# Kernel optimization log

Hardware: AMD Instinct MI355X
Metric: run time of the kernel (lower is better)

The kernel has to match this reference:

```python
import jax, jax.numpy as jnp
import numpy as np

EMBED = 512
NH = 8
HD = EMBED // NH
NL = 12
FFN = 2048
TD = 16  # latent_channels * patch_size**2 = 4*4


def _ln(x, g, b):
    m = x.mean(-1, keepdims=True)
    v = ((x - m) ** 2).mean(-1, keepdims=True)
    return (x - m) * jax.lax.rsqrt(v + 1e-5) * g + b


def _pos_emb(H, W, d):
    # faithful to get_2d_rope_embedding: cosine 1D embeddings along h and w, concatenated
    dh = d // 2
    inv = 1.0 / (10000.0 ** (jnp.arange(dh, dtype=jnp.float32) / dh))
    peh = jnp.cos(jnp.arange(H, dtype=jnp.float32)[:, None] * inv[None, :])  # (H, dh)
    pew = jnp.cos(jnp.arange(W, dtype=jnp.float32)[:, None] * inv[None, :])  # (W, dh)
    pe = jnp.concatenate([
        jnp.broadcast_to(peh[:, None, :], (H, W, dh)),
        jnp.broadcast_to(pew[None, :, :], (H, W, dh)),
    ], axis=-1)
    return pe.reshape(H * W, d)


def setup_inputs() -> dict:
    key = jax.random.key(0)
    ks = jax.random.split(key, 20)
    B, L = 8, 1024
    s = 0.02
    inp = {
        'x': jax.random.normal(ks[0], (B, L, TD), jnp.float32),
        'token_mask': jnp.ones((B, L), jnp.int32),
        'W_in': s * jax.random.normal(ks[1], (TD, EMBED), jnp.float32),
        'b_in': jnp.zeros((EMBED,), jnp.float32),
        'ln1_g': jnp.ones((NL, EMBED), jnp.float32),
        'ln1_b': jnp.zeros((NL, EMBED), jnp.float32),
        'Wq': s * jax.random.normal(ks[2], (NL, EMBED, EMBED), jnp.float32),
        'Wk': s * jax.random.normal(ks[3], (NL, EMBED, EMBED), jnp.float32),
        'Wv': s * jax.random.normal(ks[4], (NL, EMBED, EMBED), jnp.float32),
        'Wo': s * jax.random.normal(ks[5], (NL, EMBED, EMBED), jnp.float32),
        'ln2_g': jnp.ones((NL, EMBED), jnp.float32),
        'ln2_b': jnp.zeros((NL, EMBED), jnp.float32),
        'W1': s * jax.random.normal(ks[6], (NL, EMBED, FFN), jnp.float32),
        'W2': s * jax.random.normal(ks[7], (NL, EMBED, FFN), jnp.float32),
        'W3': s * jax.random.normal(ks[8], (NL, FFN, EMBED), jnp.float32),
        'W_out': s * jax.random.normal(ks[9], (EMBED, TD), jnp.float32),
        'b_out': jnp.zeros((TD,), jnp.float32),
        'H': 32,
        'W': 32,
    }
    return inp


def reference(x, token_mask, W_in, b_in, ln1_g, ln1_b, Wq, Wk, Wv, Wo,
              ln2_g, ln2_b, W1, W2, W3, W_out, b_out, H, W):
    B, L, _ = x.shape
    scale = 1.0 / np.sqrt(HD).astype(np.float32)
    h = x @ W_in + b_in + _pos_emb(H, W, EMBED)[None]  # (B, L, E)
    # (B,1,1,L) additive mask, -1e9 at padded positions
    mask = (token_mask == 0)[:, None, None, :].astype(h.dtype) * (-1e9)

    def block(h, p):
        g1, b1, wq, wk, wv, wo, g2, b2, w1, w2, w3 = p
        xn = _ln(h, g1, b1)
        q = (xn @ wq).reshape(B, L, NH, HD)
        k = (xn @ wk).reshape(B, L, NH, HD)
        v = (xn @ wv).reshape(B, L, NH, HD)
        s = jnp.einsum('blhd,bmhd->bhlm', q, k) * scale + mask
        a = jax.nn.softmax(s, axis=-1)
        o = jnp.einsum('bhlm,bmhd->blhd', a, v).reshape(B, L, EMBED) @ wo
        h = h + o
        xn = _ln(h, g2, b2)
        h = h + (jax.nn.silu(xn @ w1) * (xn @ w2)) @ w3
        return h, None

    h, _ = jax.lax.scan(block, h, (ln1_g, ln1_b, Wq, Wk, Wv, Wo, ln2_g, ln2_b, W1, W2, W3))
    return h @ W_out + b_out  # (B, L, TD)
```

## Files before the change

kernel.cpp:

```cpp
#include <hip/hip_runtime.h>

typedef __attribute__((ext_vector_type(8))) short short8;
typedef __attribute__((ext_vector_type(4))) float f32x4;
typedef __attribute__((ext_vector_type(4))) unsigned short us4;

#define MFMA_BF16(a,b,c) __builtin_amdgcn_mfma_f32_16x16x32_bf16((a),(b),(c),0,0,0)

__device__ __forceinline__ unsigned short f2bf(float f) {
  unsigned int u = __float_as_uint(f);
  u += 0x7fffu + ((u >> 16) & 1u);
  return (unsigned short)(u >> 16);
}

__global__ __launch_bounds__(256) void wtrans_kernel(const float* __restrict__ src,
                                                     unsigned short* __restrict__ dst,
                                                     int R, int C) {
  __shared__ float tile[32][33];
  int c0 = blockIdx.x * 32, r0 = blockIdx.y * 32;
  const float* s = src + (size_t)blockIdx.z * R * C;
  unsigned short* d = dst + (size_t)blockIdx.z * R * C;
  int tx = threadIdx.x, ty = threadIdx.y;
#pragma unroll
  for (int i = 0; i < 32; i += 8)
    tile[ty + i][tx] = s[(size_t)(r0 + ty + i) * C + c0 + tx];
  __syncthreads();
#pragma unroll
  for (int i = 0; i < 32; i += 8)
    d[(size_t)(c0 + ty + i) * R + r0 + tx] = f2bf(tile[tx][ty + i]);
}

__global__ __launch_bounds__(128) void embed_kernel(const float* __restrict__ x,
                                                    const float* __restrict__ Win,
                                                    const float* __restrict__ bin,
                                                    float* __restrict__ h) {
  __shared__ float xs[16];
  int m = blockIdx.x, t = threadIdx.x;
  if (t < 16) xs[t] = x[m * 16 + t];
  __syncthreads();
  int l = m & 1023, hi = l >> 5, wi = l & 31;
#pragma unroll
  for (int e0 = 0; e0 < 512; e0 += 128) {
    int e = e0 + t;
    float a = bin[e];
#pragma unroll
    for (int kk = 0; kk < 16; kk++) a += xs[kk] * Win[kk * 512 + e];
    int j = e & 255;
    float p = (e < 256) ? (float)hi : (float)wi;
    float inv = expf((float)j * (-9.210340371976184f / 256.0f));
    a += cosf(p * inv);
    h[(size_t)m * 512 + e] = a;
  }
}

__global__ __launch_bounds__(128) void ln_kernel(const float* __restrict__ h,
                                                 const float* __restrict__ gw,
                                                 const float* __restrict__ bw,
                                                 unsigned short* __restrict__ xn) {
  int m = blockIdx.x, t = threadIdx.x;
  f32x4 v = *(const f32x4*)&h[(size_t)m * 512 + t * 4];
  float s = v[0] + v[1] + v[2] + v[3];
  float q = v[0]*v[0] + v[1]*v[1] + v[2]*v[2] + v[3]*v[3];
#pragma unroll
  for (int o = 1; o < 64; o <<= 1) { s += __shfl_xor(s, o); q += __shfl_xor(q, o); }
  __shared__ float red[4];
  if ((t & 63) == 0) { red[(t >> 6) * 2] = s; red[(t >> 6) * 2 + 1] = q; }
  __syncthreads();
  s = red[0] + red[2]; q = red[1] + red[3];
  float mean = s * (1.0f / 512.0f);
  float var = q * (1.0f / 512.0f) - mean * mean;
  float rstd = rsqrtf(var + 1e-5f);
  f32x4 gg = *(const f32x4*)&gw[t * 4];
  f32x4 bb = *(const f32x4*)&bw[t * 4];
  us4 w;
#pragma unroll
  for (int r = 0; r < 4; r++) w[r] = f2bf((v[r] - mean) * rstd * gg[r] + bb[r]);
  *(us4*)&xn[(size_t)m * 512 + t * 4] = w;
}

__global__ __launch_bounds__(256) void qkv_gemm(const unsigned short* __restrict__ xn,
                                                const unsigned short* __restrict__ wtq,
                                                const unsigned short* __restrict__ wtk,
                                                const unsigned short* __restrict__ wtv,
                                                unsigned short* __restrict__ qo,
                                                unsigned short* __restrict__ ko,
                                                unsigned short* __restrict__ vo) {
  __shared__ short8 As[512];
  __shared__ short8 Bs[512];
  int n0 = blockIdx.x * 128, m0 = blockIdx.y * 128;
  int sel = n0 >> 9;
  const short8* wt = (const short8*)(sel == 0 ? wtq : sel == 1 ? wtk : wtv);
  unsigned short* out = sel == 0 ? qo : sel == 1 ? ko : vo;
  int nw = n0 & 511;
  const short8* A8 = (const short8*)xn;
  int tid = threadIdx.x, wid = tid >> 6, lane = tid & 63;
  int wr = wid >> 1, wc = wid & 1, c16 = lane & 15, g = lane >> 4;
  int subA = wid * 2;
  f32x4 acc[4][4] = {};
  short8 ra[2], rb[2];
#pragma unroll
  for (int s = 0; s < 2; s++) {
    ra[s] = A8[(size_t)(m0 + (subA + s) * 16 + c16) * 64 + g];
    rb[s] = wt[(size_t)(nw + (subA + s) * 16 + c16) * 64 + g];
  }
  for (int kt = 0; kt < 16; kt++) {
    __syncthreads();
#pragma unroll
    for (int s = 0; s < 2; s++) {
      As[(subA + s) * 64 + lane] = ra[s];
      Bs[(subA + s) * 64 + lane] = rb[s];
    }
    if (kt < 15) {
#pragma unroll
      for (int s = 0; s < 2; s++) {
        ra[s] = A8[(size_t)(m0 + (subA + s) * 16 + c16) * 64 + (kt + 1) * 4 + g];
        rb[s] = wt[(size_t)(nw + (subA + s) * 16 + c16) * 64 + (kt + 1) * 4 + g];
      }
    }
    __syncthreads();
    short8 af[4], bf[4];
#pragma unroll
    for (int mf = 0; mf < 4; mf++) af[mf] = As[(wr * 4 + mf) * 64 + lane];
#pragma unroll
    for (int nf = 0; nf < 4; nf++) bf[nf] = Bs[(wc * 4 + nf) * 64 + lane];
#pragma unroll
    for (int mf = 0; mf < 4; mf++)
#pragma unroll
      for (int nf = 0; nf < 4; nf++)
        acc[mf][nf] = MFMA_BF16(af[mf], bf[nf], acc[mf][nf]);
  }
#pragma unroll
  for (int mf = 0; mf < 4; mf++)
#pragma unroll
    for (int nf = 0; nf < 4; nf++) {
      int col = nw + wc * 64 + nf * 16 + c16;
#pragma unroll
      for (int r = 0; r < 4; r++) {
        int row = m0 + wr * 64 + mf * 16 + g * 4 + r;
        out[(size_t)row * 512 + col] = f2bf(acc[mf][nf][r]);
      }
    }
}

__global__ __launch_bounds__(256) void gemm_res(const unsigned short* __restrict__ A,
                                                const unsigned short* __restrict__ Wt,
                                                float* __restrict__ h, int Kd8, int nkt) {
  __shared__ short8 As[512];
  __shared__ short8 Bs[512];
  int n0 = blockIdx.x * 128, m0 = blockIdx.y * 128;
  const short8* A8 = (const short8*)A;
  const short8* W8 = (const short8*)Wt;
  int tid = threadIdx.x, wid = tid >> 6, lane = tid & 63;
  int wr = wid >> 1, wc = wid & 1, c16 = lane & 15, g = lane >> 4;
  int subA = wid * 2;
  f32x4 acc[4][4] = {};
  short8 ra[2], rb[2];
#pragma unroll
  for (int s = 0; s < 2; s++) {
    ra[s] = A8[(size_t)(m0 + (subA + s) * 16 + c16) * Kd8 + g];
    rb[s] = W8[(size_t)(n0 + (subA + s) * 16 + c16) * Kd8 + g];
  }
  for (int kt = 0; kt < nkt; kt++) {
    __syncthreads();
#pragma unroll
    for (int s = 0; s < 2; s++) {
      As[(subA + s) * 64 + lane] = ra[s];
      Bs[(subA + s) * 64 + lane] = rb[s];
    }
    if (kt + 1 < nkt) {
#pragma unroll
      for (int s = 0; s < 2; s++) {
        ra[s] = A8[(size_t)(m0 + (subA + s) * 16 + c16) * Kd8 + (kt + 1) * 4 + g];
        rb[s] = W8[(size_t)(n0 + (subA + s) * 16 + c16) * Kd8 + (kt + 1) * 4 + g];
      }
    }
    __syncthreads();
    short8 af[4], bf[4];
#pragma unroll
    for (int mf = 0; mf < 4; mf++) af[mf] = As[(wr * 4 + mf) * 64 + lane];
#pragma unroll
    for (int nf = 0; nf < 4; nf++) bf[nf] = Bs[(wc * 4 + nf) * 64 + lane];
#pragma unroll
    for (int mf = 0; mf < 4; mf++)
#pragma unroll
      for (int nf = 0; nf < 4; nf++)
        acc[mf][nf] = MFMA_BF16(af[mf], bf[nf], acc[mf][nf]);
  }
#pragma unroll
  for (int mf = 0; mf < 4; mf++)
#pragma unroll
    for (int nf = 0; nf < 4; nf++) {
      int col = n0 + wc * 64 + nf * 16 + c16;
#pragma unroll
      for (int r = 0; r < 4; r++) {
        int row = m0 + wr * 64 + mf * 16 + g * 4 + r;
        h[(size_t)row * 512 + col] += acc[mf][nf][r];
      }
    }
}

__global__ __launch_bounds__(256) void ffn_gemm(const unsigned short* __restrict__ xn,
                                                const unsigned short* __restrict__ w1t,
                                                const unsigned short* __restrict__ w2t,
                                                unsigned short* __restrict__ gout) {
  __shared__ short8 As[512];
  __shared__ short8 B1s[512];
  __shared__ short8 B2s[512];
  int n0 = blockIdx.x * 128, m0 = blockIdx.y * 128;
  const short8* A8 = (const short8*)xn;
  const short8* W18 = (const short8*)w1t;
  const short8* W28 = (const short8*)w2t;
  int tid = threadIdx.x, wid = tid >> 6, lane = tid & 63;
  int wr = wid >> 1, wc = wid & 1, c16 = lane & 15, g = lane >> 4;
  int subA = wid * 2;
  f32x4 acc1[4][4] = {};
  f32x4 acc2[4][4] = {};
  short8 ra[2], rb1[2], rb2[2];
#pragma unroll
  for (int s = 0; s < 2; s++) {
    ra[s]  = A8 [(size_t)(m0 + (subA + s) * 16 + c16) * 64 + g];
    rb1[s] = W18[(size_t)(n0 + (subA + s) * 16 + c16) * 64 + g];
    rb2[s] = W28[(size_t)(n0 + (subA + s) * 16 + c16) * 64 + g];
  }
  for (int kt = 0; kt < 16; kt++) {
    __syncthreads();
#pragma unroll
    for (int s = 0; s < 2; s++) {
      As [(subA + s) * 64 + lane] = ra[s];
      B1s[(subA + s) * 64 + lane] = rb1[s];
      B2s[(subA + s) * 64 + lane] = rb2[s];
    }
    if (kt < 15) {
#pragma unroll
      for (int s = 0; s < 2; s++) {
        ra[s]  = A8 [(size_t)(m0 + (subA + s) * 16 + c16) * 64 + (kt + 1) * 4 + g];
        rb1[s] = W18[(size_t)(n0 + (subA + s) * 16 + c16) * 64 + (kt + 1) * 4 + g];
        rb2[s] = W28[(size_t)(n0 + (subA + s) * 16 + c16) * 64 + (kt + 1) * 4 + g];
      }
    }
    __syncthreads();
    short8 af[4], b1f[4], b2f[4];
#pragma unroll
    for (int mf = 0; mf < 4; mf++) af[mf] = As[(wr * 4 + mf) * 64 + lane];
#pragma unroll
    for (int nf = 0; nf < 4; nf++) {
      b1f[nf] = B1s[(wc * 4 + nf) * 64 + lane];
      b2f[nf] = B2s[(wc * 4 + nf) * 64 + lane];
    }
#pragma unroll
    for (int mf = 0; mf < 4; mf++)
#pragma unroll
      for (int nf = 0; nf < 4; nf++) {
        acc1[mf][nf] = MFMA_BF16(af[mf], b1f[nf], acc1[mf][nf]);
        acc2[mf][nf] = MFMA_BF16(af[mf], b2f[nf], acc2[mf][nf]);
      }
  }
#pragma unroll
  for (int mf = 0; mf < 4; mf++)
#pragma unroll
    for (int nf = 0; nf < 4; nf++) {
      int col = n0 + wc * 64 + nf * 16 + c16;
#pragma unroll
      for (int r = 0; r < 4; r++) {
        int row = m0 + wr * 64 + mf * 16 + g * 4 + r;
        float xx = acc1[mf][nf][r];
        float yy = acc2[mf][nf][r];
        float sg = xx / (1.0f + __expf(-xx));
        gout[(size_t)row * 2048 + col] = f2bf(sg * yy);
      }
    }
}

__global__ __launch_bounds__(256) void vtrans_kernel(const unsigned short* __restrict__ v,
                                                     unsigned short* __restrict__ vt) {
  __shared__ __align__(16) unsigned short tile[64][72];
  int bid = blockIdx.x;
  int bh = bid >> 4, lt = bid & 15;
  int b = bh >> 3, hh = bh & 7;
  int t = threadIdx.x;
  int lr = t >> 2, d0 = (t & 3) * 16;
  const unsigned short* src = v + (size_t)(b * 1024 + lt * 64 + lr) * 512 + hh * 64 + d0;
  *(short8*)&tile[lr][d0] = *(const short8*)src;
  *(short8*)&tile[lr][d0 + 8] = *(const short8*)(src + 8);
  __syncthreads();
  int d = t & 63, l0 = (t >> 6) * 16;
  unsigned short* dst = vt + (size_t)(bh * 64 + d) * 1024 + lt * 64 + l0;
  short8 w0, w1;
#pragma unroll
  for (int i = 0; i < 8; i++) w0[i] = (short)tile[l0 + i][d];
#pragma unroll
  for (int i = 0; i < 8; i++) w1[i] = (short)tile[l0 + 8 + i][d];
  *(short8*)dst = w0;
  *(short8*)(dst + 8) = w1;
}

__global__ __launch_bounds__(256) void attn_kernel(const unsigned short* __restrict__ q,
                                                   const unsigned short* __restrict__ k,
                                                   const unsigned short* __restrict__ vt,
                                                   const int* __restrict__ tmsk,
                                                   unsigned short* __restrict__ o) {
  __shared__ short8 Ks[512];
  __shared__ short8 Vs[512];
  __shared__ uint2  Pb[2048];
  __shared__ f32x4  maskv[256];

  int bid = blockIdx.x;
  int qb = bid & 7;
  int bh = bid >> 3;
  int b = bh >> 3, hh = bh & 7;
  int tid = threadIdx.x, wid = tid >> 6, lane = tid & 63;
  int c16 = lane & 15, gq = lane >> 4;
  int qrow0 = qb * 128 + wid * 32;

  const short8* q8 = (const short8*)q;
  const short8* k8 = (const short8*)k;
  const short8* v8 = (const short8*)vt;

  short8 qf[2][2];
#pragma unroll
  for (int nf = 0; nf < 2; nf++)
#pragma unroll
    for (int dc = 0; dc < 2; dc++)
      qf[nf][dc] = q8[(size_t)(b * 1024 + qrow0 + nf * 16 + c16) * 64 + hh * 8 + dc * 4 + gq];

  {
    int4 mm = ((const int4*)(tmsk + b * 1024))[tid];
    f32x4 ma;
    ma[0] = (mm.x == 0) ? -1e9f : 0.0f;
    ma[1] = (mm.y == 0) ? -1e9f : 0.0f;
    ma[2] = (mm.z == 0) ? -1e9f : 0.0f;
    ma[3] = (mm.w == 0) ? -1e9f : 0.0f;
    maskv[tid] = ma;
  }

  short8 rk[2], rv[2];
#pragma unroll
  for (int s = 0; s < 2; s++) {
    int sub = wid * 2 + s;
    rk[s] = k8[(size_t)(b * 1024 + (sub >> 1) * 16 + c16) * 64 + hh * 8 + (sub & 1) * 4 + gq];
    rv[s] = v8[(size_t)(bh * 64 + (sub >> 1) * 16 + c16) * 128 + (sub & 1) * 4 + gq];
  }

  float mrun[2] = {-1e30f, -1e30f};
  float lrun[2] = {0.0f, 0.0f};
  f32x4 accO[4][2] = {};

  for (int kt = 0; kt < 16; kt++) {
    __syncthreads();
#pragma unroll
    for (int s = 0; s < 2; s++) {
      int sub = wid * 2 + s;
      Ks[sub * 64 + lane] = rk[s];
      Vs[sub * 64 + lane] = rv[s];
    }
    if (kt < 15) {
      int kt2 = kt + 1;
#pragma unroll
      for (int s = 0; s < 2; s++) {
        int sub = wid * 2 + s;
        rk[s] = k8[(size_t)(b * 1024 + kt2 * 64 + (sub >> 1) * 16 + c16) * 64 + hh * 8 + (sub & 1) * 4 + gq];
        rv[s] = v8[(size_t)(bh * 64 + (sub >> 1) * 16 + c16) * 128 + kt2 * 8 + (sub & 1) * 4 + gq];
      }
    }
    __syncthreads();

    f32x4 sT[4][2] = {};
#pragma unroll
    for (int mf = 0; mf < 4; mf++) {
      short8 ka0 = Ks[(mf * 2 + 0) * 64 + lane];
      short8 ka1 = Ks[(mf * 2 + 1) * 64 + lane];
#pragma unroll
      for (int nf = 0; nf < 2; nf++) {
        sT[mf][nf] = MFMA_BF16(ka0, qf[nf][0], sT[mf][nf]);
        sT[mf][nf] = MFMA_BF16(ka1, qf[nf][1], sT[mf][nf]);
      }
    }

#pragma unroll
    for (int nf = 0; nf < 2; nf++) {
      float pv[4][4];
      float tm = -1e30f;
#pragma unroll
      for (int mf = 0; mf < 4; mf++) {
        f32x4 mk = maskv[kt * 16 + mf * 4 + gq];
#pragma unroll
        for (int r = 0; r < 4; r++) {
          float sv = sT[mf][nf][r] * 0.125f + mk[r];
          pv[mf][r] = sv;
          tm = fmaxf(tm, sv);
        }
      }
      tm = fmaxf(tm, __shfl_xor(tm, 16));
      tm = fmaxf(tm, __shfl_xor(tm, 32));
      float mn = fmaxf(mrun[nf], tm);
      float fac = __expf(mrun[nf] - mn);
      mrun[nf] = mn;
      float ts = 0.0f;
#pragma unroll
      for (int mf = 0; mf < 4; mf++)
#pragma unroll
        for (int r = 0; r < 4; r++) {
          float p = __expf(pv[mf][r] - mn);
          pv[mf][r] = p;
          ts += p;
        }
      ts += __shfl_xor(ts, 16);
      ts += __shfl_xor(ts, 32);
      lrun[nf] = lrun[nf] * fac + ts;
#pragma unroll
      for (int dmf = 0; dmf < 4; dmf++) accO[dmf][nf] *= fac;
#pragma unroll
      for (int mf = 0; mf < 4; mf++) {
        unsigned lo = (unsigned)f2bf(pv[mf][0]) | ((unsigned)f2bf(pv[mf][1]) << 16);
        unsigned hi = (unsigned)f2bf(pv[mf][2]) | ((unsigned)f2bf(pv[mf][3]) << 16);
        int kk = mf >> 1;
        int gr = (mf & 1) * 2 + (gq >> 1);
        uint2 t2; t2.x = lo; t2.y = hi;
        Pb[wid * 512 + ((nf * 2 + kk) * 64 + gr * 16 + c16) * 2 + (gq & 1)] = t2;
      }
    }
    __syncthreads();

    const short8* Pb8 = (const short8*)Pb;
#pragma unroll
    for (int nf = 0; nf < 2; nf++) {
      short8 pb0 = Pb8[wid * 256 + (nf * 2 + 0) * 64 + lane];
      short8 pb1 = Pb8[wid * 256 + (nf * 2 + 1) * 64 + lane];
#pragma unroll
      for (int dmf = 0; dmf < 4; dmf++) {
        short8 va0 = Vs[(dmf * 2 + 0) * 64 + lane];
        short8 va1 = Vs[(dmf * 2 + 1) * 64 + lane];
        accO[dmf][nf] = MFMA_BF16(va0, pb0, accO[dmf][nf]);
        accO[dmf][nf] = MFMA_BF16(va1, pb1, accO[dmf][nf]);
      }
    }
  }

#pragma unroll
  for (int nf = 0; nf < 2; nf++) {
    float inv = 1.0f / lrun[nf];
    int row = b * 1024 + qrow0 + nf * 16 + c16;
#pragma unroll
    for (int dmf = 0; dmf < 4; dmf++) {
      us4 w;
#pragma unroll
      for (int r = 0; r < 4; r++) w[r] = f2bf(accO[dmf][nf][r] * inv);
      *(us4*)&o[(size_t)row * 512 + hh * 64 + dmf * 16 + gq * 4] = w;
    }
  }
}

__global__ __launch_bounds__(128) void out_kernel(const float* __restrict__ h,
                                                  const float* __restrict__ Wout,
                                                  const float* __restrict__ bout,
                                                  float* __restrict__ out) {
  __shared__ f32x4 hs4[8][128];
  __shared__ f32x4 Ws4[16][129];
  int t = threadIdx.x;
  int rb = blockIdx.x * 8;
  float* hsf = (float*)hs4;
  float* wsf = (float*)Ws4;
  for (int i = t; i < 4096; i += 128) hsf[i] = h[(size_t)rb * 512 + i];
  for (int i = t; i < 8192; i += 128) wsf[(i & 15) * 516 + (i >> 4)] = Wout[i];
  __syncthreads();
  int r = t >> 4, c = t & 15;
  float acc = bout[c];
  for (int k4 = 0; k4 < 128; k4++) {
    f32x4 a = hs4[r][k4];
    f32x4 w = Ws4[c][k4];
    acc += a[0]*w[0] + a[1]*w[1] + a[2]*w[2] + a[3]*w[3];
  }
  out[(rb + r) * 16 + c] = acc;
}

extern "C" void kernel_launch(void* const* d_in, const int* in_sizes, int n_in,
                              void* d_out, int out_size, void* d_ws, size_t ws_size,
                              hipStream_t stream) {
  const float* x    = (const float*)d_in[0];
  const int*   tmsk = (const int*)d_in[1];
  const float* Win  = (const float*)d_in[2];
  const float* bin  = (const float*)d_in[3];
  const float* ln1g = (const float*)d_in[4];
  const float* ln1b = (const float*)d_in[5];
  const float* Wq   = (const float*)d_in[6];
  const float* Wk   = (const float*)d_in[7];
  const float* Wv   = (const float*)d_in[8];
  const float* Wo   = (const float*)d_in[9];
  const float* ln2g = (const float*)d_in[10];
  const float* ln2b = (const float*)d_in[11];
  const float* W1   = (const float*)d_in[12];
  const float* W2   = (const float*)d_in[13];
  const float* W3   = (const float*)d_in[14];
  const float* Wout = (const float*)d_in[15];
  const float* bout = (const float*)d_in[16];
  float* outp = (float*)d_out;

  char* ws = (char*)d_ws;
  unsigned short* wtq = (unsigned short*)(ws + 0);
  unsigned short* wtk = (unsigned short*)(ws + 6291456);
  unsigned short* wtv = (unsigned short*)(ws + 12582912);
  unsigned short* wto = (unsigned short*)(ws + 18874368);
  unsigned short* wt1 = (unsigned short*)(ws + 25165824);
  unsigned short* wt2 = (unsigned short*)(ws + 50331648);
  unsigned short* wt3 = (unsigned short*)(ws + 75497472);
  float*          h   = (float*)(ws + 100663296);
  unsigned short* xn  = (unsigned short*)(ws + 117440512);
  unsigned short* qb  = (unsigned short*)(ws + 125829120);
  unsigned short* kb  = (unsigned short*)(ws + 134217728);
  unsigned short* vb  = (unsigned short*)(ws + 142606336);
  unsigned short* vtb = (unsigned short*)(ws + 150994944);
  unsigned short* ob  = (unsigned short*)(ws + 159383552);
  unsigned short* gb  = (unsigned short*)(ws + 167772160);

  dim3 tb(32, 8);
  wtrans_kernel<<<dim3(16, 16, 12), tb, 0, stream>>>(Wq, wtq, 512, 512);
  wtrans_kernel<<<dim3(16, 16, 12), tb, 0, stream>>>(Wk, wtk, 512, 512);
  wtrans_kernel<<<dim3(16, 16, 12), tb, 0, stream>>>(Wv, wtv, 512, 512);
  wtrans_kernel<<<dim3(16, 16, 12), tb, 0, stream>>>(Wo, wto, 512, 512);
  wtrans_kernel<<<dim3(64, 16, 12), tb, 0, stream>>>(W1, wt1, 512, 2048);
  wtrans_kernel<<<dim3(64, 16, 12), tb, 0, stream>>>(W2, wt2, 512, 2048);
  wtrans_kernel<<<dim3(16, 64, 12), tb, 0, stream>>>(W3, wt3, 2048, 512);

  embed_kernel<<<8192, 128, 0, stream>>>(x, Win, bin, h);

  for (int l = 0; l < 12; l++) {
    ln_kernel<<<8192, 128, 0, stream>>>(h, ln1g + l * 512, ln1b + l * 512, xn);
    qkv_gemm<<<dim3(12, 64), 256, 0, stream>>>(xn,
        wtq + (size_t)l * 262144, wtk + (size_t)l * 262144, wtv + (size_t)l * 262144,
        qb, kb, vb);
    vtrans_kernel<<<1024, 256, 0, stream>>>(vb, vtb);
    attn_kernel<<<512, 256, 0, stream>>>(qb, kb, vtb, tmsk, ob);
    gemm_res<<<dim3(4, 64), 256, 0, stream>>>(ob, wto + (size_t)l * 262144, h, 64, 16);
    ln_kernel<<<8192, 128, 0, stream>>>(h, ln2g + l * 512, ln2b + l * 512, xn);
    ffn_gemm<<<dim3(16, 64), 256, 0, stream>>>(xn,
        wt1 + (size_t)l * 1048576, wt2 + (size_t)l * 1048576, gb);
    gemm_res<<<dim3(4, 64), 256, 0, stream>>>(gb, wt3 + (size_t)l * 1048576, h, 256, 64);
  }
  out_kernel<<<1024, 128, 0, stream>>>(h, Wout, bout, outp);

  (void)in_sizes; (void)n_in; (void)out_size; (void)ws_size;
}
```

Baseline: 2.720 ms.

## Double-buffer GEMM tiles via direct global-to-LDS async loads

The three MFMA GEMM kernels (QKV, residual, FFN) now load tiles straight from global memory into LDS with global_load_lds, instead of staging them through registers. LDS is double-buffered so the next k-tile is fetched while the current one feeds the MFMAs. This cuts register staging and one barrier per iteration. In exchange it doubles LDS use, which may lower occupancy. It also relies on the compiler's waitcnt handling before each barrier to make the async LDS writes visible.

```diff
diff --git a/kernel.cpp b/kernel.cpp
--- a/kernel.cpp
+++ b/kernel.cpp
@@ -5,6 +5,13 @@
 typedef __attribute__((ext_vector_type(4))) unsigned short us4;
 
 #define MFMA_BF16(a,b,c) __builtin_amdgcn_mfma_f32_16x16x32_bf16((a),(b),(c),0,0,0)
+
+typedef __attribute__((address_space(3))) void* lds_vp;
+typedef const __attribute__((address_space(1))) void* gbl_vp;
+
+__device__ __forceinline__ void gl16(const void* g, void* l) {
+  __builtin_amdgcn_global_load_lds((gbl_vp)g, (lds_vp)l, 16, 0, 0);
+}
 
 __device__ __forceinline__ unsigned short f2bf(float f) {
   unsigned int u = __float_as_uint(f);
@@ -84,8 +91,8 @@
                                                 unsigned short* __restrict__ qo,
                                                 unsigned short* __restrict__ ko,
                                                 unsigned short* __restrict__ vo) {
-  __shared__ short8 As[512];
-  __shared__ short8 Bs[512];
+  __shared__ short8 As[2][512];
+  __shared__ short8 Bs[2][512];
   int n0 = blockIdx.x * 128, m0 = blockIdx.y * 128;
   int sel = n0 >> 9;
   const short8* wt = (const short8*)(sel == 0 ? wtq : sel == 1 ? wtk : wtv);
@@ -94,39 +101,39 @@
   const short8* A8 = (const short8*)xn;
   int tid = threadIdx.x, wid = tid >> 6, lane = tid & 63;
   int wr = wid >> 1, wc = wid & 1, c16 = lane & 15, g = lane >> 4;
-  int subA = wid * 2;
+  int sub0 = wid * 2, sub1 = wid * 2 + 1;
+  const short8* aS0 = A8 + (size_t)(m0 + sub0 * 16 + c16) * 64 + g;
+  const short8* aS1 = A8 + (size_t)(m0 + sub1 * 16 + c16) * 64 + g;
+  const short8* bS0 = wt + (size_t)(nw + sub0 * 16 + c16) * 64 + g;
+  const short8* bS1 = wt + (size_t)(nw + sub1 * 16 + c16) * 64 + g;
   f32x4 acc[4][4] = {};
-  short8 ra[2], rb[2];
-#pragma unroll
-  for (int s = 0; s < 2; s++) {
-    ra[s] = A8[(size_t)(m0 + (subA + s) * 16 + c16) * 64 + g];
-    rb[s] = wt[(size_t)(nw + (subA + s) * 16 + c16) * 64 + g];
-  }
+
+  gl16(aS0, &As[0][sub0 * 64]);
+  gl16(aS1, &As[0][sub1 * 64]);
+  gl16(bS0, &Bs[0][sub0 * 64]);
+  gl16(bS1, &Bs[0][sub1 * 64]);
+  __syncthreads();
+  int cur = 0;
   for (int kt = 0; kt < 16; kt++) {
-    __syncthreads();
-#pragma unroll
-    for (int s = 0; s < 2; s++) {
-      As[(subA + s) * 64 + lane] = ra[s];
-      Bs[(subA + s) * 64 + lane] = rb[s];
-    }
     if (kt < 15) {
-#pragma unroll
-      for (int s = 0; s < 2; s++) {
-        ra[s] = A8[(size_t)(m0 + (subA + s) * 16 + c16) * 64 + (kt + 1) * 4 + g];
-        rb[s] = wt[(size_t)(nw + (subA + s) * 16 + c16) * 64 + (kt + 1) * 4 + g];
-      }
-    }
-    __syncthreads();
+      int ko_ = (kt + 1) * 4;
+      gl16(aS0 + ko_, &As[cur ^ 1][sub0 * 64]);
+      gl16(aS1 + ko_, &As[cur ^ 1][sub1 * 64]);
+      gl16(bS0 + ko_, &Bs[cur ^ 1][sub0 * 64]);
+      gl16(bS1 + ko_, &Bs[cur ^ 1][sub1 * 64]);
+    }
     short8 af[4], bf[4];
 #pragma unroll
-    for (int mf = 0; mf < 4; mf++) af[mf] = As[(wr * 4 + mf) * 64 + lane];
-#pragma unroll
-    for (int nf = 0; nf < 4; nf++) bf[nf] = Bs[(wc * 4 + nf) * 64 + lane];
+    for (int mf = 0; mf < 4; mf++) af[mf] = As[cur][(wr * 4 + mf) * 64 + lane];
+#pragma unroll
+    for (int nf = 0; nf < 4; nf++) bf[nf] = Bs[cur][(wc * 4 + nf) * 64 + lane];
 #pragma unroll
     for (int mf = 0; mf < 4; mf++)
 #pragma unroll
       for (int nf = 0; nf < 4; nf++)
         acc[mf][nf] = MFMA_BF16(af[mf], bf[nf], acc[mf][nf]);
+    __syncthreads();
+    cur ^= 1;
   }
 #pragma unroll
   for (int mf = 0; mf < 4; mf++)
@@ -144,46 +151,46 @@
 __global__ __launch_bounds__(256) void gemm_res(const unsigned short* __restrict__ A,
                                                 const unsigned short* __restrict__ Wt,
                                                 float* __restrict__ h, int Kd8, int nkt) {
-  __shared__ short8 As[512];
-  __shared__ short8 Bs[512];
+  __shared__ short8 As[2][512];
+  __shared__ short8 Bs[2][512];
   int n0 = blockIdx.x * 128, m0 = blockIdx.y * 128;
   const short8* A8 = (const short8*)A;
   const short8* W8 = (const short8*)Wt;
   int tid = threadIdx.x, wid = tid >> 6, lane = tid & 63;
   int wr = wid >> 1, wc = wid & 1, c16 = lane & 15, g = lane >> 4;
-  int subA = wid * 2;
+  int sub0 = wid * 2, sub1 = wid * 2 + 1;
+  const short8* aS0 = A8 + (size_t)(m0 + sub0 * 16 + c16) * Kd8 + g;
+  const short8* aS1 = A8 + (size_t)(m0 + sub1 * 16 + c16) * Kd8 + g;
+  const short8* bS0 = W8 + (size_t)(n0 + sub0 * 16 + c16) * Kd8 + g;
+  const short8* bS1 = W8 + (size_t)(n0 + sub1 * 16 + c16) * Kd8 + g;
   f32x4 acc[4][4] = {};
-  short8 ra[2], rb[2];
-#pragma unroll
-  for (int s = 0; s < 2; s++) {
-    ra[s] = A8[(size_t)(m0 + (subA + s) * 16 + c16) * Kd8 + g];
-    rb[s] = W8[(size_t)(n0 + (subA + s) * 16 + c16) * Kd8 + g];
-  }
+
+  gl16(aS0, &As[0][sub0 * 64]);
+  gl16(aS1, &As[0][sub1 * 64]);
+  gl16(bS0, &Bs[0][sub0 * 64]);
+  gl16(bS1, &Bs[0][sub1 * 64]);
+  __syncthreads();
+  int cur = 0;
   for (int kt = 0; kt < nkt; kt++) {
-    __syncthreads();
-#pragma unroll
-    for (int s = 0; s < 2; s++) {
-      As[(subA + s) * 64 + lane] = ra[s];
-      Bs[(subA + s) * 64 + lane] = rb[s];
-    }
     if (kt + 1 < nkt) {
-#pragma unroll
-      for (int s = 0; s < 2; s++) {
-        ra[s] = A8[(size_t)(m0 + (subA + s) * 16 + c16) * Kd8 + (kt + 1) * 4 + g];
-        rb[s] = W8[(size_t)(n0 + (subA + s) * 16 + c16) * Kd8 + (kt + 1) * 4 + g];
-      }
-    }
-    __syncthreads();
+      int ko_ = (kt + 1) * 4;
+      gl16(aS0 + ko_, &As[cur ^ 1][sub0 * 64]);
+      gl16(aS1 + ko_, &As[cur ^ 1][sub1 * 64]);
+      gl16(bS0 + ko_, &Bs[cur ^ 1][sub0 * 64]);
+      gl16(bS1 + ko_, &Bs[cur ^ 1][sub1 * 64]);
+    }
     short8 af[4], bf[4];
 #pragma unroll
-    for (int mf = 0; mf < 4; mf++) af[mf] = As[(wr * 4 + mf) * 64 + lane];
-#pragma unroll
-    for (int nf = 0; nf < 4; nf++) bf[nf] = Bs[(wc * 4 + nf) * 64 + lane];
+    for (int mf = 0; mf < 4; mf++) af[mf] = As[cur][(wr * 4 + mf) * 64 + lane];
+#pragma unroll
+    for (int nf = 0; nf < 4; nf++) bf[nf] = Bs[cur][(wc * 4 + nf) * 64 + lane];
 #pragma unroll
     for (int mf = 0; mf < 4; mf++)
 #pragma unroll
       for (int nf = 0; nf < 4; nf++)
         acc[mf][nf] = MFMA_BF16(af[mf], bf[nf], acc[mf][nf]);
+    __syncthreads();
+    cur ^= 1;
   }
 #pragma unroll
   for (int mf = 0; mf < 4; mf++)
@@ -202,49 +209,50 @@
                                                 const unsigned short* __restrict__ w1t,
                                                 const unsigned short* __restrict__ w2t,
                                                 unsigned short* __restrict__ gout) {
-  __shared__ short8 As[512];
-  __shared__ short8 B1s[512];
-  __shared__ short8 B2s[512];
+  __shared__ short8 As[2][512];
+  __shared__ short8 B1s[2][512];
+  __shared__ short8 B2s[2][512];
   int n0 = blockIdx.x * 128, m0 = blockIdx.y * 128;
   const short8* A8 = (const short8*)xn;
   const short8* W18 = (const short8*)w1t;
   const short8* W28 = (const short8*)w2t;
   int tid = threadIdx.x, wid = tid >> 6, lane = tid & 63;
   int wr = wid >> 1, wc = wid & 1, c16 = lane & 15, g = lane >> 4;
-  int subA = wid * 2;
+  int sub0 = wid * 2, sub1 = wid * 2 + 1;
+  const short8* aS0 = A8 + (size_t)(m0 + sub0 * 16 + c16) * 64 + g;
+  const short8* aS1 = A8 + (size_t)(m0 + sub1 * 16 + c16) * 64 + g;
+  const short8* b1S0 = W18 + (size_t)(n0 + sub0 * 16 + c16) * 64 + g;
+  const short8* b1S1 = W18 + (size_t)(n0 + sub1 * 16 + c16) * 64 + g;
+  const short8* b2S0 = W28 + (size_t)(n0 + sub0 * 16 + c16) * 64 + g;
+  const short8* b2S1 = W28 + (size_t)(n0 + sub1 * 16 + c16) * 64 + g;
   f32x4 acc1[4][4] = {};
   f32x4 acc2[4][4] = {};
-  short8 ra[2], rb1[2], rb2[2];
-#pragma unroll
-  for (int s = 0; s < 2; s++) {
-    ra[s]  = A8 [(size_t)(m0 + (subA + s) * 16 + c16) * 64 + g];
-    rb1[s] = W18[(size_t)(n0 + (subA + s) * 16 + c16) * 64 + g];
-    rb2[s] = W28[(size_t)(n0 + (subA + s) * 16 + c16) * 64 + g];
-  }
+
+  gl16(aS0, &As[0][sub0 * 64]);
+  gl16(aS1, &As[0][sub1 * 64]);
+  gl16(b1S0, &B1s[0][sub0 * 64]);
+  gl16(b1S1, &B1s[0][sub1 * 64]);
+  gl16(b2S0, &B2s[0][sub0 * 64]);
+  gl16(b2S1, &B2s[0][sub1 * 64]);
+  __syncthreads();
+  int cur = 0;
   for (int kt = 0; kt < 16; kt++) {
-    __syncthreads();
-#pragma unroll
-    for (int s = 0; s < 2; s++) {
-      As [(subA + s) * 64 + lane] = ra[s];
-      B1s[(subA + s) * 64 + lane] = rb1[s];
-      B2s[(subA + s) * 64 + lane] = rb2[s];
-    }
     if (kt < 15) {
-#pragma unroll
-      for (int s = 0; s < 2; s++) {
-        ra[s]  = A8 [(size_t)(m0 + (subA + s) * 16 + c16) * 64 + (kt + 1) * 4 + g];
-        rb1[s] = W18[(size_t)(n0 + (subA + s) * 16 + c16) * 64 + (kt + 1) * 4 + g];
-        rb2[s] = W28[(size_t)(n0 + (subA + s) * 16 + c16) * 64 + (kt + 1) * 4 + g];
-      }
-    }
-    __syncthreads();
+      int ko_ = (kt + 1) * 4;
+      gl16(aS0 + ko_, &As[cur ^ 1][sub0 * 64]);
+      gl16(aS1 + ko_, &As[cur ^ 1][sub1 * 64]);
+      gl16(b1S0 + ko_, &B1s[cur ^ 1][sub0 * 64]);
+      gl16(b1S1 + ko_, &B1s[cur ^ 1][sub1 * 64]);
+      gl16(b2S0 + ko_, &B2s[cur ^ 1][sub0 * 64]);
+      gl16(b2S1 + ko_, &B2s[cur ^ 1][sub1 * 64]);
+    }
     short8 af[4], b1f[4], b2f[4];
 #pragma unroll
-    for (int mf = 0; mf < 4; mf++) af[mf] = As[(wr * 4 + mf) * 64 + lane];
+    for (int mf = 0; mf < 4; mf++) af[mf] = As[cur][(wr * 4 + mf) * 64 + lane];
 #pragma unroll
     for (int nf = 0; nf < 4; nf++) {
-      b1f[nf] = B1s[(wc * 4 + nf) * 64 + lane];
-      b2f[nf] = B2s[(wc * 4 + nf) * 64 + lane];
+      b1f[nf] = B1s[cur][(wc * 4 + nf) * 64 + lane];
+      b2f[nf] = B2s[cur][(wc * 4 + nf) * 64 + lane];
     }
 #pragma unroll
     for (int mf = 0; mf < 4; mf++)
@@ -253,6 +261,8 @@
         acc1[mf][nf] = MFMA_BF16(af[mf], b1f[nf], acc1[mf][nf]);
         acc2[mf][nf] = MFMA_BF16(af[mf], b2f[nf], acc2[mf][nf]);
       }
+    __syncthreads();
+    cur ^= 1;
   }
 #pragma unroll
   for (int mf = 0; mf < 4; mf++)
```

Result: slower. 3.053 ms (+12.2%).

## Use direct global-to-LDS loads with K=64 tiles and narrower residual GEMM tiles

Applied to the files above, without the earlier changes.

The three GEMM kernels now load tiles with global_load_lds straight into shared memory, skipping the register staging. The K tile doubles to 64, which halves the number of barrier pairs per K step. The residual GEMMs use 128x64 output tiles, doubling their grid to 512 blocks for better CU occupancy. The register prefetch overlap is dropped, so load latency is now exposed between barriers, and LDS use per block grows.

```diff
diff --git a/kernel.cpp b/kernel.cpp
--- a/kernel.cpp
+++ b/kernel.cpp
@@ -5,6 +5,13 @@
 typedef __attribute__((ext_vector_type(4))) unsigned short us4;
 
 #define MFMA_BF16(a,b,c) __builtin_amdgcn_mfma_f32_16x16x32_bf16((a),(b),(c),0,0,0)
+
+typedef __attribute__((address_space(3))) void* lds_vp;
+typedef const __attribute__((address_space(1))) void* gbl_vp;
+
+__device__ __forceinline__ void gl16(const void* g, void* l) {
+  __builtin_amdgcn_global_load_lds((gbl_vp)g, (lds_vp)l, 16, 0, 0);
+}
 
 __device__ __forceinline__ unsigned short f2bf(float f) {
   unsigned int u = __float_as_uint(f);
@@ -84,8 +91,8 @@
                                                 unsigned short* __restrict__ qo,
                                                 unsigned short* __restrict__ ko,
                                                 unsigned short* __restrict__ vo) {
-  __shared__ short8 As[512];
-  __shared__ short8 Bs[512];
+  __shared__ short8 As[1024];
+  __shared__ short8 Bs[1024];
   int n0 = blockIdx.x * 128, m0 = blockIdx.y * 128;
   int sel = n0 >> 9;
   const short8* wt = (const short8*)(sel == 0 ? wtq : sel == 1 ? wtk : wtv);
@@ -94,39 +101,36 @@
   const short8* A8 = (const short8*)xn;
   int tid = threadIdx.x, wid = tid >> 6, lane = tid & 63;
   int wr = wid >> 1, wc = wid & 1, c16 = lane & 15, g = lane >> 4;
-  int subA = wid * 2;
+  const short8* aSrc[4];
+  const short8* bSrc[4];
+#pragma unroll
+  for (int s = 0; s < 4; s++) {
+    int sub = wid * 4 + s, rg = sub >> 1, kc = sub & 1;
+    aSrc[s] = A8 + (size_t)(m0 + rg * 16 + c16) * 64 + kc * 4 + g;
+    bSrc[s] = wt + (size_t)(nw + rg * 16 + c16) * 64 + kc * 4 + g;
+  }
   f32x4 acc[4][4] = {};
-  short8 ra[2], rb[2];
-#pragma unroll
-  for (int s = 0; s < 2; s++) {
-    ra[s] = A8[(size_t)(m0 + (subA + s) * 16 + c16) * 64 + g];
-    rb[s] = wt[(size_t)(nw + (subA + s) * 16 + c16) * 64 + g];
-  }
-  for (int kt = 0; kt < 16; kt++) {
+  for (int kt = 0; kt < 8; kt++) {
+    if (kt) __syncthreads();
+#pragma unroll
+    for (int s = 0; s < 4; s++) {
+      gl16(aSrc[s] + kt * 8, &As[(wid * 4 + s) * 64]);
+      gl16(bSrc[s] + kt * 8, &Bs[(wid * 4 + s) * 64]);
+    }
     __syncthreads();
 #pragma unroll
-    for (int s = 0; s < 2; s++) {
-      As[(subA + s) * 64 + lane] = ra[s];
-      Bs[(subA + s) * 64 + lane] = rb[s];
-    }
-    if (kt < 15) {
-#pragma unroll
-      for (int s = 0; s < 2; s++) {
-        ra[s] = A8[(size_t)(m0 + (subA + s) * 16 + c16) * 64 + (kt + 1) * 4 + g];
-        rb[s] = wt[(size_t)(nw + (subA + s) * 16 + c16) * 64 + (kt + 1) * 4 + g];
-      }
-    }
-    __syncthreads();
-    short8 af[4], bf[4];
-#pragma unroll
-    for (int mf = 0; mf < 4; mf++) af[mf] = As[(wr * 4 + mf) * 64 + lane];
-#pragma unroll
-    for (int nf = 0; nf < 4; nf++) bf[nf] = Bs[(wc * 4 + nf) * 64 + lane];
-#pragma unroll
-    for (int mf = 0; mf < 4; mf++)
-#pragma unroll
-      for (int nf = 0; nf < 4; nf++)
-        acc[mf][nf] = MFMA_BF16(af[mf], bf[nf], acc[mf][nf]);
+    for (int kc = 0; kc < 2; kc++) {
+      short8 af[4], bf[4];
+#pragma unroll
+      for (int mf = 0; mf < 4; mf++) af[mf] = As[((wr * 4 + mf) * 2 + kc) * 64 + lane];
+#pragma unroll
+      for (int nf = 0; nf < 4; nf++) bf[nf] = Bs[((wc * 4 + nf) * 2 + kc) * 64 + lane];
+#pragma unroll
+      for (int mf = 0; mf < 4; mf++)
+#pragma unroll
+        for (int nf = 0; nf < 4; nf++)
+          acc[mf][nf] = MFMA_BF16(af[mf], bf[nf], acc[mf][nf]);
+    }
   }
 #pragma unroll
   for (int mf = 0; mf < 4; mf++)
@@ -144,52 +148,52 @@
 __global__ __launch_bounds__(256) void gemm_res(const unsigned short* __restrict__ A,
                                                 const unsigned short* __restrict__ Wt,
                                                 float* __restrict__ h, int Kd8, int nkt) {
-  __shared__ short8 As[512];
+  __shared__ short8 As[1024];
   __shared__ short8 Bs[512];
-  int n0 = blockIdx.x * 128, m0 = blockIdx.y * 128;
+  int n0 = blockIdx.x * 64, m0 = blockIdx.y * 128;
   const short8* A8 = (const short8*)A;
   const short8* W8 = (const short8*)Wt;
   int tid = threadIdx.x, wid = tid >> 6, lane = tid & 63;
   int wr = wid >> 1, wc = wid & 1, c16 = lane & 15, g = lane >> 4;
-  int subA = wid * 2;
-  f32x4 acc[4][4] = {};
-  short8 ra[2], rb[2];
+  const short8* aSrc[4];
+  const short8* bSrc[2];
+#pragma unroll
+  for (int s = 0; s < 4; s++) {
+    int sub = wid * 4 + s, rg = sub >> 1, kc = sub & 1;
+    aSrc[s] = A8 + (size_t)(m0 + rg * 16 + c16) * Kd8 + kc * 4 + g;
+  }
 #pragma unroll
   for (int s = 0; s < 2; s++) {
-    ra[s] = A8[(size_t)(m0 + (subA + s) * 16 + c16) * Kd8 + g];
-    rb[s] = W8[(size_t)(n0 + (subA + s) * 16 + c16) * Kd8 + g];
-  }
+    int sub = wid * 2 + s, rg = sub >> 1, kc = sub & 1;
+    bSrc[s] = W8 + (size_t)(n0 + rg * 16 + c16) * Kd8 + kc * 4 + g;
+  }
+  f32x4 acc[4][2] = {};
   for (int kt = 0; kt < nkt; kt++) {
+    if (kt) __syncthreads();
+#pragma unroll
+    for (int s = 0; s < 4; s++) gl16(aSrc[s] + kt * 8, &As[(wid * 4 + s) * 64]);
+#pragma unroll
+    for (int s = 0; s < 2; s++) gl16(bSrc[s] + kt * 8, &Bs[(wid * 2 + s) * 64]);
     __syncthreads();
 #pragma unroll
-    for (int s = 0; s < 2; s++) {
-      As[(subA + s) * 64 + lane] = ra[s];
-      Bs[(subA + s) * 64 + lane] = rb[s];
-    }
-    if (kt + 1 < nkt) {
-#pragma unroll
-      for (int s = 0; s < 2; s++) {
-        ra[s] = A8[(size_t)(m0 + (subA + s) * 16 + c16) * Kd8 + (kt + 1) * 4 + g];
-        rb[s] = W8[(size_t)(n0 + (subA + s) * 16 + c16) * Kd8 + (kt + 1) * 4 + g];
-      }
-    }
-    __syncthreads();
-    short8 af[4], bf[4];
-#pragma unroll
-    for (int mf = 0; mf < 4; mf++) af[mf] = As[(wr * 4 + mf) * 64 + lane];
-#pragma unroll
-    for (int nf = 0; nf < 4; nf++) bf[nf] = Bs[(wc * 4 + nf) * 64 + lane];
-#pragma unroll
-    for (int mf = 0; mf < 4; mf++)
-#pragma unroll
-      for (int nf = 0; nf < 4; nf++)
-        acc[mf][nf] = MFMA_BF16(af[mf], bf[nf], acc[mf][nf]);
+    for (int kc = 0; kc < 2; kc++) {
+      short8 af[4], bf[2];
+#pragma unroll
+      for (int mf = 0; mf < 4; mf++) af[mf] = As[((wr * 4 + mf) * 2 + kc) * 64 + lane];
+#pragma unroll
+      for (int nf = 0; nf < 2; nf++) bf[nf] = Bs[((wc * 2 + nf) * 2 + kc) * 64 + lane];
+#pragma unroll
+      for (int mf = 0; mf < 4; mf++)
+#pragma unroll
+        for (int nf = 0; nf < 2; nf++)
+          acc[mf][nf] = MFMA_BF16(af[mf], bf[nf], acc[mf][nf]);
+    }
   }
 #pragma unroll
   for (int mf = 0; mf < 4; mf++)
 #pragma unroll
-    for (int nf = 0; nf < 4; nf++) {
-      int col = n0 + wc * 64 + nf * 16 + c16;
+    for (int nf = 0; nf < 2; nf++) {
+      int col = n0 + wc * 32 + nf * 16 + c16;
 #pragma unroll
       for (int r = 0; r < 4; r++) {
         int row = m0 + wr * 64 + mf * 16 + g * 4 + r;
@@ -202,57 +206,54 @@
                                                 const unsigned short* __restrict__ w1t,
                                                 const unsigned short* __restrict__ w2t,
                                                 unsigned short* __restrict__ gout) {
-  __shared__ short8 As[512];
-  __shared__ short8 B1s[512];
-  __shared__ short8 B2s[512];
+  __shared__ short8 As[1024];
+  __shared__ short8 B1s[1024];
+  __shared__ short8 B2s[1024];
   int n0 = blockIdx.x * 128, m0 = blockIdx.y * 128;
   const short8* A8 = (const short8*)xn;
   const short8* W18 = (const short8*)w1t;
   const short8* W28 = (const short8*)w2t;
   int tid = threadIdx.x, wid = tid >> 6, lane = tid & 63;
   int wr = wid >> 1, wc = wid & 1, c16 = lane & 15, g = lane >> 4;
-  int subA = wid * 2;
+  const short8* aSrc[4];
+  const short8* b1Src[4];
+  const short8* b2Src[4];
+#pragma unroll
+  for (int s = 0; s < 4; s++) {
+    int sub = wid * 4 + s, rg = sub >> 1, kc = sub & 1;
+    aSrc[s]  = A8  + (size_t)(m0 + rg * 16 + c16) * 64 + kc * 4 + g;
+    b1Src[s] = W18 + (size_t)(n0 + rg * 16 + c16) * 64 + kc * 4 + g;
+    b2Src[s] = W28 + (size_t)(n0 + rg * 16 + c16) * 64 + kc * 4 + g;
+  }
   f32x4 acc1[4][4] = {};
   f32x4 acc2[4][4] = {};
-  short8 ra[2], rb1[2], rb2[2];
-#pragma unroll
-  for (int s = 0; s < 2; s++) {
-    ra[s]  = A8 [(size_t)(m0 + (subA + s) * 16 + c16) * 64 + g];
-    rb1[s] = W18[(size_t)(n0 + (subA + s) * 16 + c16) * 64 + g];
-    rb2[s] = W28[(size_t)(n0 + (subA + s) * 16 + c16) * 64 + g];
-  }
-  for (int kt = 0; kt < 16; kt++) {
+  for (int kt = 0; kt < 8; kt++) {
+    if (kt) __syncthreads();
+#pragma unroll
+    for (int s = 0; s < 4; s++) {
+      gl16(aSrc[s]  + kt * 8, &As [(wid * 4 + s) * 64]);
+      gl16(b1Src[s] + kt * 8, &B1s[(wid * 4 + s) * 64]);
+      gl16(b2Src[s] + kt * 8, &B2s[(wid * 4 + s) * 64]);
+    }
     __syncthreads();
 #pragma unroll
-    for (int s = 0; s < 2; s++) {
-      As [(subA + s) * 64 + lane] = ra[s];
-      B1s[(subA + s) * 64 + lane] = rb1[s];
-      B2s[(subA + s) * 64 + lane] = rb2[s];
-    }
-    if (kt < 15) {
-#pragma unroll
-      for (int s = 0; s < 2; s++) {
-        ra[s]  = A8 [(size_t)(m0 + (subA + s) * 16 + c16) * 64 + (kt + 1) * 4 + g];
-        rb1[s] = W18[(size_t)(n0 + (subA + s) * 16 + c16) * 64 + (kt + 1) * 4 + g];
-        rb2[s] = W28[(size_t)(n0 + (subA + s) * 16 + c16) * 64 + (kt + 1) * 4 + g];
-      }
-    }
-    __syncthreads();
-    short8 af[4], b1f[4], b2f[4];
-#pragma unroll
-    for (int mf = 0; mf < 4; mf++) af[mf] = As[(wr * 4 + mf) * 64 + lane];
-#pragma unroll
-    for (int nf = 0; nf < 4; nf++) {
-      b1f[nf] = B1s[(wc * 4 + nf) * 64 + lane];
-      b2f[nf] = B2s[(wc * 4 + nf) * 64 + lane];
-    }
-#pragma unroll
-    for (int mf = 0; mf < 4; mf++)
+    for (int kc = 0; kc < 2; kc++) {
+      short8 af[4], b1f[4], b2f[4];
+#pragma unroll
+      for (int mf = 0; mf < 4; mf++) af[mf] = As[((wr * 4 + mf) * 2 + kc) * 64 + lane];
 #pragma unroll
       for (int nf = 0; nf < 4; nf++) {
-        acc1[mf][nf] = MFMA_BF16(af[mf], b1f[nf], acc1[mf][nf]);
-        acc2[mf][nf] = MFMA_BF16(af[mf], b2f[nf], acc2[mf][nf]);
-      }
+        b1f[nf] = B1s[((wc * 4 + nf) * 2 + kc) * 64 + lane];
+        b2f[nf] = B2s[((wc * 4 + nf) * 2 + kc) * 64 + lane];
+      }
+#pragma unroll
+      for (int mf = 0; mf < 4; mf++)
+#pragma unroll
+        for (int nf = 0; nf < 4; nf++) {
+          acc1[mf][nf] = MFMA_BF16(af[mf], b1f[nf], acc1[mf][nf]);
+          acc2[mf][nf] = MFMA_BF16(af[mf], b2f[nf], acc2[mf][nf]);
+        }
+    }
   }
 #pragma unroll
   for (int mf = 0; mf < 4; mf++)
@@ -529,11 +530,11 @@
         qb, kb, vb);
     vtrans_kernel<<<1024, 256, 0, stream>>>(vb, vtb);
     attn_kernel<<<512, 256, 0, stream>>>(qb, kb, vtb, tmsk, ob);
-    gemm_res<<<dim3(4, 64), 256, 0, stream>>>(ob, wto + (size_t)l * 262144, h, 64, 16);
+    gemm_res<<<dim3(8, 64), 256, 0, stream>>>(ob, wto + (size_t)l * 262144, h, 64, 8);
     ln_kernel<<<8192, 128, 0, stream>>>(h, ln2g + l * 512, ln2b + l * 512, xn);
     ffn_gemm<<<dim3(16, 64), 256, 0, stream>>>(xn,
         wt1 + (size_t)l * 1048576, wt2 + (size_t)l * 1048576, gb);
-    gemm_res<<<dim3(4, 64), 256, 0, stream>>>(gb, wt3 + (size_t)l * 1048576, h, 256, 64);
+    gemm_res<<<dim3(8, 64), 256, 0, stream>>>(gb, wt3 + (size_t)l * 1048576, h, 256, 32);
   }
   out_kernel<<<1024, 128, 0, stream>>>(h, Wout, bout, outp);
 
```

After: 3.173 ms. 1.17x slower.

## Load GEMM fragments directly from global memory, dropping LDS staging and barriers

Applied to the files above, without the earlier changes.

The three MFMA GEMM kernels (qkv, residual, FFN) no longer stage A/B tiles through shared memory with register prefetch and two barriers per k-step. Each wave now reads its own MFMA fragments straight from global memory via precomputed row pointers, with partial loop unrolling and launch_bounds requesting two blocks per CU. This removes LDS traffic and synchronisation, but each fragment is now fetched by two waves (data sharing across waves moves to the L1/L2 caches), the loads are strided 16-byte reads, and the software prefetch that overlapped loads with MFMA is lost.

```diff
diff --git a/kernel.cpp b/kernel.cpp
--- a/kernel.cpp
+++ b/kernel.cpp
@@ -77,15 +77,13 @@
   *(us4*)&xn[(size_t)m * 512 + t * 4] = w;
 }
 
-__global__ __launch_bounds__(256) void qkv_gemm(const unsigned short* __restrict__ xn,
-                                                const unsigned short* __restrict__ wtq,
-                                                const unsigned short* __restrict__ wtk,
-                                                const unsigned short* __restrict__ wtv,
-                                                unsigned short* __restrict__ qo,
-                                                unsigned short* __restrict__ ko,
-                                                unsigned short* __restrict__ vo) {
-  __shared__ short8 As[512];
-  __shared__ short8 Bs[512];
+__global__ __launch_bounds__(256, 2) void qkv_gemm(const unsigned short* __restrict__ xn,
+                                                   const unsigned short* __restrict__ wtq,
+                                                   const unsigned short* __restrict__ wtk,
+                                                   const unsigned short* __restrict__ wtv,
+                                                   unsigned short* __restrict__ qo,
+                                                   unsigned short* __restrict__ ko,
+                                                   unsigned short* __restrict__ vo) {
   int n0 = blockIdx.x * 128, m0 = blockIdx.y * 128;
   int sel = n0 >> 9;
   const short8* wt = (const short8*)(sel == 0 ? wtq : sel == 1 ? wtk : wtv);
@@ -94,34 +92,20 @@
   const short8* A8 = (const short8*)xn;
   int tid = threadIdx.x, wid = tid >> 6, lane = tid & 63;
   int wr = wid >> 1, wc = wid & 1, c16 = lane & 15, g = lane >> 4;
-  int subA = wid * 2;
+  const short8* aB[4];
+  const short8* bB[4];
+#pragma unroll
+  for (int mf = 0; mf < 4; mf++) aB[mf] = A8 + (size_t)(m0 + (wr * 4 + mf) * 16 + c16) * 64 + g;
+#pragma unroll
+  for (int nf = 0; nf < 4; nf++) bB[nf] = wt + (size_t)(nw + (wc * 4 + nf) * 16 + c16) * 64 + g;
   f32x4 acc[4][4] = {};
-  short8 ra[2], rb[2];
-#pragma unroll
-  for (int s = 0; s < 2; s++) {
-    ra[s] = A8[(size_t)(m0 + (subA + s) * 16 + c16) * 64 + g];
-    rb[s] = wt[(size_t)(nw + (subA + s) * 16 + c16) * 64 + g];
-  }
+#pragma unroll 4
   for (int kt = 0; kt < 16; kt++) {
-    __syncthreads();
-#pragma unroll
-    for (int s = 0; s < 2; s++) {
-      As[(subA + s) * 64 + lane] = ra[s];
-      Bs[(subA + s) * 64 + lane] = rb[s];
-    }
-    if (kt < 15) {
-#pragma unroll
-      for (int s = 0; s < 2; s++) {
-        ra[s] = A8[(size_t)(m0 + (subA + s) * 16 + c16) * 64 + (kt + 1) * 4 + g];
-        rb[s] = wt[(size_t)(nw + (subA + s) * 16 + c16) * 64 + (kt + 1) * 4 + g];
-      }
-    }
-    __syncthreads();
     short8 af[4], bf[4];
 #pragma unroll
-    for (int mf = 0; mf < 4; mf++) af[mf] = As[(wr * 4 + mf) * 64 + lane];
-#pragma unroll
-    for (int nf = 0; nf < 4; nf++) bf[nf] = Bs[(wc * 4 + nf) * 64 + lane];
+    for (int mf = 0; mf < 4; mf++) af[mf] = aB[mf][kt * 4];
+#pragma unroll
+    for (int nf = 0; nf < 4; nf++) bf[nf] = bB[nf][kt * 4];
 #pragma unroll
     for (int mf = 0; mf < 4; mf++)
 #pragma unroll
@@ -141,44 +125,28 @@
     }
 }
 
-__global__ __launch_bounds__(256) void gemm_res(const unsigned short* __restrict__ A,
-                                                const unsigned short* __restrict__ Wt,
-                                                float* __restrict__ h, int Kd8, int nkt) {
-  __shared__ short8 As[512];
-  __shared__ short8 Bs[512];
+__global__ __launch_bounds__(256, 2) void gemm_res(const unsigned short* __restrict__ A,
+                                                   const unsigned short* __restrict__ Wt,
+                                                   float* __restrict__ h, int Kd8, int nkt) {
   int n0 = blockIdx.x * 128, m0 = blockIdx.y * 128;
   const short8* A8 = (const short8*)A;
   const short8* W8 = (const short8*)Wt;
   int tid = threadIdx.x, wid = tid >> 6, lane = tid & 63;
   int wr = wid >> 1, wc = wid & 1, c16 = lane & 15, g = lane >> 4;
-  int subA = wid * 2;
+  const short8* aB[4];
+  const short8* bB[4];
+#pragma unroll
+  for (int mf = 0; mf < 4; mf++) aB[mf] = A8 + (size_t)(m0 + (wr * 4 + mf) * 16 + c16) * Kd8 + g;
+#pragma unroll
+  for (int nf = 0; nf < 4; nf++) bB[nf] = W8 + (size_t)(n0 + (wc * 4 + nf) * 16 + c16) * Kd8 + g;
   f32x4 acc[4][4] = {};
-  short8 ra[2], rb[2];
-#pragma unroll
-  for (int s = 0; s < 2; s++) {
-    ra[s] = A8[(size_t)(m0 + (subA + s) * 16 + c16) * Kd8 + g];
-    rb[s] = W8[(size_t)(n0 + (subA + s) * 16 + c16) * Kd8 + g];
-  }
+#pragma unroll 4
   for (int kt = 0; kt < nkt; kt++) {
-    __syncthreads();
-#pragma unroll
-    for (int s = 0; s < 2; s++) {
-      As[(subA + s) * 64 + lane] = ra[s];
-      Bs[(subA + s) * 64 + lane] = rb[s];
-    }
-    if (kt + 1 < nkt) {
-#pragma unroll
-      for (int s = 0; s < 2; s++) {
-        ra[s] = A8[(size_t)(m0 + (subA + s) * 16 + c16) * Kd8 + (kt + 1) * 4 + g];
-        rb[s] = W8[(size_t)(n0 + (subA + s) * 16 + c16) * Kd8 + (kt + 1) * 4 + g];
-      }
-    }
-    __syncthreads();
     short8 af[4], bf[4];
 #pragma unroll
-    for (int mf = 0; mf < 4; mf++) af[mf] = As[(wr * 4 + mf) * 64 + lane];
-#pragma unroll
-    for (int nf = 0; nf < 4; nf++) bf[nf] = Bs[(wc * 4 + nf) * 64 + lane];
+    for (int mf = 0; mf < 4; mf++) af[mf] = aB[mf][kt * 4];
+#pragma unroll
+    for (int nf = 0; nf < 4; nf++) bf[nf] = bB[nf][kt * 4];
 #pragma unroll
     for (int mf = 0; mf < 4; mf++)
 #pragma unroll
@@ -198,54 +166,35 @@
     }
 }
 
-__global__ __launch_bounds__(256) void ffn_gemm(const unsigned short* __restrict__ xn,
-                                                const unsigned short* __restrict__ w1t,
-                                                const unsigned short* __restrict__ w2t,
-                                                unsigned short* __restrict__ gout) {
-  __shared__ short8 As[512];
-  __shared__ short8 B1s[512];
-  __shared__ short8 B2s[512];
+__global__ __launch_bounds__(256, 2) void ffn_gemm(const unsigned short* __restrict__ xn,
+                                                   const unsigned short* __restrict__ w1t,
+                                                   const unsigned short* __restrict__ w2t,
+                                                   unsigned short* __restrict__ gout) {
   int n0 = blockIdx.x * 128, m0 = blockIdx.y * 128;
   const short8* A8 = (const short8*)xn;
   const short8* W18 = (const short8*)w1t;
   const short8* W28 = (const short8*)w2t;
   int tid = threadIdx.x, wid = tid >> 6, lane = tid & 63;
   int wr = wid >> 1, wc = wid & 1, c16 = lane & 15, g = lane >> 4;
-  int subA = wid * 2;
+  const short8* aB[4];
+  const short8* b1B[4];
+  const short8* b2B[4];
+#pragma unroll
+  for (int mf = 0; mf < 4; mf++) aB[mf] = A8 + (size_t)(m0 + (wr * 4 + mf) * 16 + c16) * 64 + g;
+#pragma unroll
+  for (int nf = 0; nf < 4; nf++) {
+    b1B[nf] = W18 + (size_t)(n0 + (wc * 4 + nf) * 16 + c16) * 64 + g;
+    b2B[nf] = W28 + (size_t)(n0 + (wc * 4 + nf) * 16 + c16) * 64 + g;
+  }
   f32x4 acc1[4][4] = {};
   f32x4 acc2[4][4] = {};
-  short8 ra[2], rb1[2], rb2[2];
-#pragma unroll
-  for (int s = 0; s < 2; s++) {
-    ra[s]  = A8 [(size_t)(m0 + (subA + s) * 16 + c16) * 64 + g];
-    rb1[s] = W18[(size_t)(n0 + (subA + s) * 16 + c16) * 64 + g];
-    rb2[s] = W28[(size_t)(n0 + (subA + s) * 16 + c16) * 64 + g];
-  }
+#pragma unroll 2
   for (int kt = 0; kt < 16; kt++) {
-    __syncthreads();
-#pragma unroll
-    for (int s = 0; s < 2; s++) {
-      As [(subA + s) * 64 + lane] = ra[s];
-      B1s[(subA + s) * 64 + lane] = rb1[s];
-      B2s[(subA + s) * 64 + lane] = rb2[s];
-    }
-    if (kt < 15) {
-#pragma unroll
-      for (int s = 0; s < 2; s++) {
-        ra[s]  = A8 [(size_t)(m0 + (subA + s) * 16 + c16) * 64 + (kt + 1) * 4 + g];
-        rb1[s] = W18[(size_t)(n0 + (subA + s) * 16 + c16) * 64 + (kt + 1) * 4 + g];
-        rb2[s] = W28[(size_t)(n0 + (subA + s) * 16 + c16) * 64 + (kt + 1) * 4 + g];
-      }
-    }
-    __syncthreads();
     short8 af[4], b1f[4], b2f[4];
 #pragma unroll
-    for (int mf = 0; mf < 4; mf++) af[mf] = As[(wr * 4 + mf) * 64 + lane];
-#pragma unroll
-    for (int nf = 0; nf < 4; nf++) {
-      b1f[nf] = B1s[(wc * 4 + nf) * 64 + lane];
-      b2f[nf] = B2s[(wc * 4 + nf) * 64 + lane];
-    }
+    for (int mf = 0; mf < 4; mf++) af[mf] = aB[mf][kt * 4];
+#pragma unroll
+    for (int nf = 0; nf < 4; nf++) { b1f[nf] = b1B[nf][kt * 4]; b2f[nf] = b2B[nf][kt * 4]; }
 #pragma unroll
     for (int mf = 0; mf < 4; mf++)
 #pragma unroll
```

Measured after the change: 3.653 ms. 34.3% more time.
